# Kernel optimization log

Measured on AMD Instinct MI355X. Metric: run time of the kernel, lower is better.

Reference implementation:

```python
import jax, jax.numpy as jnp
import numpy as np

Q_MAX = 127.0  # 2**(8-1) - 1

def _quant_per_tensor_absmax(t):
    # scale = clamp(absmax, 1e-5) / 127 ; q = round(t / scale)
    scale = jnp.maximum(jnp.max(jnp.abs(t)), 1e-5) / Q_MAX
    q = jnp.round(t / scale)
    return q, scale

def setup_inputs() -> dict:
    key = jax.random.key(0)
    k1, k2, k3 = jax.random.split(key, 3)
    B, S, IN, OUT = 4, 2048, 4096, 4096
    x = jax.random.normal(k1, (B, S, IN), dtype=jnp.float32)
    weight = jax.random.normal(k2, (OUT, IN), dtype=jnp.float32)
    bias = jax.random.normal(k3, (1, OUT), dtype=jnp.float32)
    return {"x": x, "weight": weight, "bias": bias}

def reference(x, weight, bias):
    # per-tensor weight quantization (done at from_float time in the original)
    q_w, s_w = _quant_per_tensor_absmax(weight)   # q_w: [OUT, IN] integer-valued
    # per-tensor activation quantization (forward path)
    q_x, s_x = _quant_per_tensor_absmax(x)        # q_x: [B, S, IN] integer-valued
    # int8 GEMM (simulated in fp32: values are small integers) + fused dequant
    y = jnp.einsum('bsi,oi->bso', q_x, q_w)       # [B, S, OUT]
    y = y * (s_x * s_w) + bias                    # dequant scale + bias
    return y
```

## Files before the change

### kernel.cpp

```cpp
#include <hip/hip_runtime.h>
#include <hip/hip_bf16.h>
#include <stdint.h>

#define M_DIM 8192
#define N_DIM 4096
#define K_DIM 4096

typedef int i32x4 __attribute__((ext_vector_type(4)));

#define NB_X 2048
#define NB_W 1024
#define NB_TOT (NB_X + NB_W)

__global__ void w8a8_absmax_kernel(const float* __restrict__ x,
                                   const float* __restrict__ w,
                                   float* __restrict__ partials) {
    int b = blockIdx.x;
    const float4* p;
    int n8, bi, nb;
    if (b < NB_X) { p = (const float4*)x; n8 = (M_DIM * K_DIM) / 8; bi = b;        nb = NB_X; }
    else          { p = (const float4*)w; n8 = (N_DIM * K_DIM) / 8; bi = b - NB_X; nb = NB_W; }

    float m = 0.f;
    int stride = nb * 256;
    for (int i = bi * 256 + threadIdx.x; i < n8; i += stride) {
        float4 v0 = p[2 * i];
        float4 v1 = p[2 * i + 1];
        float m0 = fmaxf(fmaxf(fabsf(v0.x), fabsf(v0.y)), fmaxf(fabsf(v0.z), fabsf(v0.w)));
        float m1 = fmaxf(fmaxf(fabsf(v1.x), fabsf(v1.y)), fmaxf(fabsf(v1.z), fabsf(v1.w)));
        m = fmaxf(m, fmaxf(m0, m1));
    }
    #pragma unroll
    for (int o = 32; o > 0; o >>= 1)
        m = fmaxf(m, __shfl_xor(m, o, 64));

    __shared__ float red[4];
    if ((threadIdx.x & 63) == 0) red[threadIdx.x >> 6] = m;
    __syncthreads();
    if (threadIdx.x == 0)
        partials[b] = fmaxf(fmaxf(red[0], red[1]), fmaxf(red[2], red[3]));
}

__global__ void w8a8_finalize_kernel(const float* __restrict__ partials,
                                     float* __restrict__ finals) {
    int base = (blockIdx.x == 0) ? 0 : NB_X;
    int n    = (blockIdx.x == 0) ? NB_X : NB_W;
    float m = 0.f;
    for (int i = threadIdx.x; i < n; i += 256)
        m = fmaxf(m, partials[base + i]);
    #pragma unroll
    for (int o = 32; o > 0; o >>= 1)
        m = fmaxf(m, __shfl_xor(m, o, 64));
    __shared__ float red[4];
    if ((threadIdx.x & 63) == 0) red[threadIdx.x >> 6] = m;
    __syncthreads();
    if (threadIdx.x == 0) {
        m = fmaxf(fmaxf(red[0], red[1]), fmaxf(red[2], red[3]));
        finals[blockIdx.x] = fmaxf(m, 1e-5f) / 127.0f;
    }
}

__global__ void w8a8_quant_kernel(const float* __restrict__ x,
                                  const float* __restrict__ w,
                                  uint2* __restrict__ qx,
                                  uint2* __restrict__ qw,
                                  const float* __restrict__ finals) {
    int b = blockIdx.x;
    const float4* in4;
    uint2* outq;
    int n8, bi, nb;
    float scale;
    if (b < NB_X) { in4 = (const float4*)x; outq = qx; n8 = (M_DIM * K_DIM) / 8; bi = b;        nb = NB_X; scale = finals[0]; }
    else          { in4 = (const float4*)w; outq = qw; n8 = (N_DIM * K_DIM) / 8; bi = b - NB_X; nb = NB_W; scale = finals[1]; }

    int stride = nb * 256;
    for (int i = bi * 256 + threadIdx.x; i < n8; i += stride) {
        float4 v0 = in4[2 * i];
        float4 v1 = in4[2 * i + 1];
        int a0 = (int)rintf(v0.x / scale), a1 = (int)rintf(v0.y / scale);
        int a2 = (int)rintf(v0.z / scale), a3 = (int)rintf(v0.w / scale);
        int a4 = (int)rintf(v1.x / scale), a5 = (int)rintf(v1.y / scale);
        int a6 = (int)rintf(v1.z / scale), a7 = (int)rintf(v1.w / scale);
        uint2 o;
        o.x = (unsigned)(a0 & 0xff) | ((unsigned)(a1 & 0xff) << 8) |
              ((unsigned)(a2 & 0xff) << 16) | ((unsigned)(a3 & 0xff) << 24);
        o.y = (unsigned)(a4 & 0xff) | ((unsigned)(a5 & 0xff) << 8) |
              ((unsigned)(a6 & 0xff) << 16) | ((unsigned)(a7 & 0xff) << 24);
        outq[i] = o;
    }
}

#define BM 256
#define BN 256
#define BK 128
#define NT (K_DIM / BK)
#define NTN (N_DIM / BN)
#define LDS_BUF 65536

#define STAGE_A(BUF, MH, KT) do {                                              \
    _Pragma("unroll")                                                          \
    for (int r_ = 0; r_ < 2; ++r_)                                             \
        __builtin_amdgcn_global_load_lds(                                      \
            (const __attribute__((address_space(1))) void*)(a_base + (size_t)((KT) + goffA[MH][r_])), \
            (__attribute__((address_space(3))) void*)(lds + (BUF)*LDS_BUF + (MH)*16384 + ldst[r_]),   \
            16, 0, 0);                                                         \
} while (0)

#define STAGE_B(BUF, NH, KT) do {                                              \
    _Pragma("unroll")                                                          \
    for (int r_ = 0; r_ < 2; ++r_)                                             \
        __builtin_amdgcn_global_load_lds(                                      \
            (const __attribute__((address_space(1))) void*)(b_base + (size_t)((KT) + goffB[NH][r_])), \
            (__attribute__((address_space(3))) void*)(lds + (BUF)*LDS_BUF + 32768 + (NH)*16384 + ldst[r_]), \
            16, 0, 0);                                                         \
} while (0)

#define RA_A(BUF, MH, DST) do {                                                \
    _Pragma("unroll")                                                          \
    for (int m4_ = 0; m4_ < 4; ++m4_) {                                        \
        DST[m4_][0] = *(const i32x4*)(lds + (BUF)*LDS_BUF + (MH)*16384 + laneA + m4_*2048 + koff[0]); \
        DST[m4_][1] = *(const i32x4*)(lds + (BUF)*LDS_BUF + (MH)*16384 + laneA + m4_*2048 + koff[1]); \
    }                                                                          \
} while (0)

#define RA_B(BUF, NH, DST) do {                                                \
    _Pragma("unroll")                                                          \
    for (int n1_ = 0; n1_ < 2; ++n1_) {                                        \
        DST[n1_][0] = *(const i32x4*)(lds + (BUF)*LDS_BUF + 32768 + (NH)*16384 + laneB + n1_*2048 + koff[0]); \
        DST[n1_][1] = *(const i32x4*)(lds + (BUF)*LDS_BUF + 32768 + (NH)*16384 + laneB + n1_*2048 + koff[1]); \
    }                                                                          \
} while (0)

#define MMA4(MH, NH, AARR, BARR) do {                                          \
    __builtin_amdgcn_s_setprio(1);                                             \
    _Pragma("unroll")                                                          \
    for (int m4_ = 0; m4_ < 4; ++m4_) {                                        \
        _Pragma("unroll")                                                      \
        for (int n1_ = 0; n1_ < 2; ++n1_) {                                    \
            i32x4 c_ = acc[(MH)*4 + m4_][(NH)*2 + n1_];                        \
            c_ = __builtin_amdgcn_mfma_i32_16x16x64_i8(AARR[m4_][0], BARR[n1_][0], c_, 0, 0, 0); \
            c_ = __builtin_amdgcn_mfma_i32_16x16x64_i8(AARR[m4_][1], BARR[n1_][1], c_, 0, 0, 0); \
            acc[(MH)*4 + m4_][(NH)*2 + n1_] = c_;                              \
        }                                                                      \
    }                                                                          \
    __builtin_amdgcn_s_setprio(0);                                             \
} while (0)

#define BAR() __builtin_amdgcn_s_barrier()
#define SB0() __builtin_amdgcn_sched_barrier(0)
#define VMW(N) asm volatile("s_waitcnt vmcnt(" #N ")" ::: "memory")
#define LGKM(N) asm volatile("s_waitcnt lgkmcnt(" #N ")" ::: "memory")

#define TILE_BODY(BUF, OBUF, KT2, B0C, B0N) do {                               \
                                              \
    RA_B(BUF, 1, bB1);                                                         \
    SB0(); LGKM(4); SB0();                   \
    MMA4(0, 0, aA0, B0C);                                                      \
    BAR();                                                                     \
              \
    STAGE_A(BUF, 0, KT2); STAGE_B(BUF, 0, KT2);                                \
    RA_A(BUF, 1, aA1);                                                         \
    SB0(); LGKM(8); SB0();                             \
    MMA4(0, 1, aA0, bB1);                                                      \
    BAR();                                                                     \
     \
    STAGE_B(BUF, 1, KT2);                                                      \
    SB0(); LGKM(0); SB0();                                        \
    MMA4(1, 1, aA1, bB1);                                                      \
    SB0(); VMW(6);                       \
    BAR();                                \
     \
    RA_A(OBUF, 0, aA0); RA_B(OBUF, 0, B0N);                                    \
    STAGE_A(BUF, 1, KT2);                                                      \
    SB0();                                       \
    MMA4(1, 0, aA1, B0C);                                                      \
    BAR();                                                                     \
} while (0)

__global__ __launch_bounds__(512, 1) void w8a8_gemm_kernel(
    const signed char* __restrict__ qa,
    const signed char* __restrict__ qb,
    const float* __restrict__ bias,
    const float* __restrict__ finals,
    float* __restrict__ out)
{
    __shared__ __align__(16) char lds[2 * LDS_BUF];

    int t    = threadIdx.x;
    int lane = t & 63;
    int wid  = t >> 6;
    int wm   = wid >> 2;
    int wn   = wid & 3;
    int fr   = lane & 15;
    int fg   = lane >> 4;
    int frb2 = (fr >> 2) & 1;

    int bid = blockIdx.x;
    int cpx = gridDim.x >> 3;
    int swz = (bid & 7) * cpx + (bid >> 3);
    int tm = swz / NTN;
    int tn = swz % NTN;

    const signed char* a_base = qa + (size_t)tm * BM * K_DIM;
    const signed char* b_base = qb + (size_t)tn * BN * K_DIM;

    int goffA[2][2], goffB[2][2], ldst[2];
    #pragma unroll
    for (int r = 0; r < 2; ++r) {
        int unit = r * 512 + t;
        int sl   = unit >> 3;
        int c    = unit & 7;
        int cs   = c ^ (sl & 7);
        int rowA = (sl & 63) + ((sl >> 6) & 1) * 128;
        goffA[0][r] = rowA * K_DIM + cs * 16;
        goffA[1][r] = (rowA + 64) * K_DIM + cs * 16;
        int rowB = ((sl >> 5) & 3) * 64 + (sl & 31);
        goffB[0][r] = rowB * K_DIM + cs * 16;
        goffB[1][r] = (rowB + 32) * K_DIM + cs * 16;
        ldst[r] = r * 8192 + t * 16;
    }

    int laneA = (wm * 64 + fr) * 128 + (fg ^ (fr & 3)) * 16;
    int laneB = (wn * 32 + fr) * 128 + (fg ^ (fr & 3)) * 16;
    int koff[2];
    koff[0] = frb2 * 64;
    koff[1] = 64 - frb2 * 64;

    i32x4 acc[8][4] = {};
    i32x4 aA0[4][2], aA1[4][2], bB1[2][2], bB0a[2][2], bB0b[2][2];

    STAGE_A(0, 0, 0);  STAGE_A(0, 1, 0);  STAGE_B(0, 0, 0);  STAGE_B(0, 1, 0);
    STAGE_A(1, 0, BK); STAGE_A(1, 1, BK); STAGE_B(1, 0, BK); STAGE_B(1, 1, BK);
    VMW(8);
    BAR();
    RA_A(0, 0, aA0); RA_B(0, 0, bB0a);

    #pragma unroll 1
    for (int it = 0; it < NT / 2; ++it) {
        int kt2 = ((2 * it + 2) & (NT - 1)) * BK;
        int kt3 = ((2 * it + 3) & (NT - 1)) * BK;
        TILE_BODY(0, 1, kt2, bB0a, bB0b);
        TILE_BODY(1, 0, kt3, bB0b, bB0a);
    }
    asm volatile("s_waitcnt vmcnt(0) lgkmcnt(0)" ::: "memory");
    BAR();

    float sprod = finals[0] * finals[1];
    int orow0 = tm * BM + wm * 128 + fg * 4;
    int ocol0 = tn * BN + wn * 64 + fr;
    #pragma unroll
    for (int n = 0; n < 4; ++n) {
        int col = ocol0 + n * 16;
        float bv = bias[col];
        #pragma unroll
        for (int m = 0; m < 8; ++m) {
            int row = orow0 + m * 16;
            #pragma unroll
            for (int rr = 0; rr < 4; ++rr) {
                out[(size_t)(row + rr) * N_DIM + col] = (float)acc[m][n][rr] * sprod + bv;
            }
        }
    }
}

extern "C" void kernel_launch(void* const* d_in, const int* in_sizes, int n_in,
                              void* d_out, int out_size, void* d_ws, size_t ws_size,
                              hipStream_t stream) {
    const float* x    = (const float*)d_in[0];
    const float* wgt  = (const float*)d_in[1];
    const float* bias = (const float*)d_in[2];
    float* out = (float*)d_out;

    char* ws = (char*)d_ws;
    float* finals   = (float*)ws;
    float* partials = (float*)(ws + 256);
    signed char* qx = (signed char*)(ws + 16384);
    signed char* qw = qx + (size_t)M_DIM * K_DIM;

    w8a8_absmax_kernel<<<NB_TOT, 256, 0, stream>>>(x, wgt, partials);
    w8a8_finalize_kernel<<<2, 256, 0, stream>>>(partials, finals);
    w8a8_quant_kernel<<<NB_TOT, 256, 0, stream>>>(x, wgt, (uint2*)qx, (uint2*)qw, finals);
    w8a8_gemm_kernel<<<(M_DIM / BM) * (N_DIM / BN), 512, 0, stream>>>(qx, qw, bias, finals, out);
}
```

Measured before the change: 216.1 us.

## Use 4 waves with 128x128 warp tiles and simplified two-phase K pipeline

Reworks the int8 GEMM from 8 waves with 128x64 per-wave tiles to 4 waves each computing a 128x128 output tile. Each wave now holds an 8x8 accumulator grid, and each half-K step is a single 64-MFMA batch. The four-phase interleaved staging schedule is replaced by a simpler one: read half-K fragments, run the MMA, barrier, stage the next tile, barrier. The aim is more register-level reuse and fewer LDS reads per MFMA, at the cost of much higher register pressure and less overlap of loads with compute.

```diff
diff --git a/kernel.cpp b/kernel.cpp
--- a/kernel.cpp
+++ b/kernel.cpp
@@ -97,51 +97,35 @@
 #define NTN (N_DIM / BN)
 #define LDS_BUF 65536
 
-#define STAGE_A(BUF, MH, KT) do {                                              \
-    _Pragma("unroll")                                                          \
-    for (int r_ = 0; r_ < 2; ++r_)                                             \
+#define STAGE_T(BUF, KT) do {                                                  \
+    _Pragma("unroll")                                                          \
+    for (int r_ = 0; r_ < 8; ++r_) {                                           \
         __builtin_amdgcn_global_load_lds(                                      \
-            (const __attribute__((address_space(1))) void*)(a_base + (size_t)((KT) + goffA[MH][r_])), \
-            (__attribute__((address_space(3))) void*)(lds + (BUF)*LDS_BUF + (MH)*16384 + ldst[r_]),   \
-            16, 0, 0);                                                         \
-} while (0)
-
-#define STAGE_B(BUF, NH, KT) do {                                              \
-    _Pragma("unroll")                                                          \
-    for (int r_ = 0; r_ < 2; ++r_)                                             \
+            (const __attribute__((address_space(1))) void*)(a_base + (size_t)(KT) + sgOff + (size_t)r_ * 131072), \
+            (__attribute__((address_space(3))) void*)(lds + (BUF)*LDS_BUF + stLds + r_*4096), 16, 0, 0); \
         __builtin_amdgcn_global_load_lds(                                      \
-            (const __attribute__((address_space(1))) void*)(b_base + (size_t)((KT) + goffB[NH][r_])), \
-            (__attribute__((address_space(3))) void*)(lds + (BUF)*LDS_BUF + 32768 + (NH)*16384 + ldst[r_]), \
-            16, 0, 0);                                                         \
-} while (0)
-
-#define RA_A(BUF, MH, DST) do {                                                \
-    _Pragma("unroll")                                                          \
-    for (int m4_ = 0; m4_ < 4; ++m4_) {                                        \
-        DST[m4_][0] = *(const i32x4*)(lds + (BUF)*LDS_BUF + (MH)*16384 + laneA + m4_*2048 + koff[0]); \
-        DST[m4_][1] = *(const i32x4*)(lds + (BUF)*LDS_BUF + (MH)*16384 + laneA + m4_*2048 + koff[1]); \
+            (const __attribute__((address_space(1))) void*)(b_base + (size_t)(KT) + sgOff + (size_t)r_ * 131072), \
+            (__attribute__((address_space(3))) void*)(lds + (BUF)*LDS_BUF + 32768 + stLds + r_*4096), 16, 0, 0); \
     }                                                                          \
 } while (0)
 
-#define RA_B(BUF, NH, DST) do {                                                \
-    _Pragma("unroll")                                                          \
-    for (int n1_ = 0; n1_ < 2; ++n1_) {                                        \
-        DST[n1_][0] = *(const i32x4*)(lds + (BUF)*LDS_BUF + 32768 + (NH)*16384 + laneB + n1_*2048 + koff[0]); \
-        DST[n1_][1] = *(const i32x4*)(lds + (BUF)*LDS_BUF + 32768 + (NH)*16384 + laneB + n1_*2048 + koff[1]); \
-    }                                                                          \
-} while (0)
-
-#define MMA4(MH, NH, AARR, BARR) do {                                          \
+#define RD_K(BUF, H, AS, BS) do {                                              \
+    _Pragma("unroll")                                                          \
+    for (int m_ = 0; m_ < 8; ++m_)                                             \
+        AS[m_] = *(const i32x4*)(lds + (BUF)*LDS_BUF + rdA + m_*2048 + koff[H]); \
+    _Pragma("unroll")                                                          \
+    for (int n_ = 0; n_ < 8; ++n_)                                             \
+        BS[n_] = *(const i32x4*)(lds + (BUF)*LDS_BUF + 32768 + rdB + n_*2048 + koff[H]); \
+} while (0)
+
+#define MMA64(AS, BS) do {                                                     \
     __builtin_amdgcn_s_setprio(1);                                             \
     _Pragma("unroll")                                                          \
-    for (int m4_ = 0; m4_ < 4; ++m4_) {                                        \
+    for (int m_ = 0; m_ < 8; ++m_) {                                           \
         _Pragma("unroll")                                                      \
-        for (int n1_ = 0; n1_ < 2; ++n1_) {                                    \
-            i32x4 c_ = acc[(MH)*4 + m4_][(NH)*2 + n1_];                        \
-            c_ = __builtin_amdgcn_mfma_i32_16x16x64_i8(AARR[m4_][0], BARR[n1_][0], c_, 0, 0, 0); \
-            c_ = __builtin_amdgcn_mfma_i32_16x16x64_i8(AARR[m4_][1], BARR[n1_][1], c_, 0, 0, 0); \
-            acc[(MH)*4 + m4_][(NH)*2 + n1_] = c_;                              \
-        }                                                                      \
+        for (int n_ = 0; n_ < 8; ++n_)                                         \
+            acc[m_][n_] = __builtin_amdgcn_mfma_i32_16x16x64_i8(               \
+                AS[m_], BS[n_], acc[m_][n_], 0, 0, 0);                         \
     }                                                                          \
     __builtin_amdgcn_s_setprio(0);                                             \
 } while (0)
@@ -151,33 +135,23 @@
 #define VMW(N) asm volatile("s_waitcnt vmcnt(" #N ")" ::: "memory")
 #define LGKM(N) asm volatile("s_waitcnt lgkmcnt(" #N ")" ::: "memory")
 
-#define TILE_BODY(BUF, OBUF, KT2, B0C, B0N) do {                               \
-                                              \
-    RA_B(BUF, 1, bB1);                                                         \
-    SB0(); LGKM(4); SB0();                   \
-    MMA4(0, 0, aA0, B0C);                                                      \
-    BAR();                                                                     \
-              \
-    STAGE_A(BUF, 0, KT2); STAGE_B(BUF, 0, KT2);                                \
-    RA_A(BUF, 1, aA1);                                                         \
-    SB0(); LGKM(8); SB0();                             \
-    MMA4(0, 1, aA0, bB1);                                                      \
-    BAR();                                                                     \
+#define TILE_BODY(X, Y, KT2) do {                                              \
      \
-    STAGE_B(BUF, 1, KT2);                                                      \
-    SB0(); LGKM(0); SB0();                                        \
-    MMA4(1, 1, aA1, bB1);                                                      \
-    SB0(); VMW(6);                       \
-    BAR();                                \
+    RD_K(X, 1, aS1, bS1);                                                      \
+    SB0(); LGKM(15); SB0();                                                    \
+    MMA64(aS0, bS0);                                                           \
      \
-    RA_A(OBUF, 0, aA0); RA_B(OBUF, 0, B0N);                                    \
-    STAGE_A(BUF, 1, KT2);                                                      \
-    SB0();                                       \
-    MMA4(1, 0, aA1, B0C);                                                      \
-    BAR();                                                                     \
-} while (0)
-
-__global__ __launch_bounds__(512, 1) void w8a8_gemm_kernel(
+    SB0(); LGKM(0); SB0();                                                     \
+    BAR();                                       \
+    STAGE_T(X, KT2);                                                           \
+    VMW(16); SB0();                  \
+    BAR();                                             \
+    RD_K(Y, 0, aS0, bS0);                                                      \
+    SB0();                                                                     \
+    MMA64(aS1, bS1);                                                           \
+} while (0)
+
+__global__ __launch_bounds__(256, 1) void w8a8_gemm_kernel(
     const signed char* __restrict__ qa,
     const signed char* __restrict__ qb,
     const float* __restrict__ bias,
@@ -189,11 +163,10 @@
     int t    = threadIdx.x;
     int lane = t & 63;
     int wid  = t >> 6;
-    int wm   = wid >> 2;
-    int wn   = wid & 3;
+    int wm   = wid >> 1;
+    int wn   = wid & 1;
     int fr   = lane & 15;
     int fg   = lane >> 4;
-    int frb2 = (fr >> 2) & 1;
 
     int bid = blockIdx.x;
     int cpx = gridDim.x >> 3;
@@ -204,52 +177,39 @@
     const signed char* a_base = qa + (size_t)tm * BM * K_DIM;
     const signed char* b_base = qb + (size_t)tn * BN * K_DIM;
 
-    int goffA[2][2], goffB[2][2], ldst[2];
-    #pragma unroll
-    for (int r = 0; r < 2; ++r) {
-        int unit = r * 512 + t;
-        int sl   = unit >> 3;
-        int c    = unit & 7;
-        int cs   = c ^ (sl & 7);
-        int rowA = (sl & 63) + ((sl >> 6) & 1) * 128;
-        goffA[0][r] = rowA * K_DIM + cs * 16;
-        goffA[1][r] = (rowA + 64) * K_DIM + cs * 16;
-        int rowB = ((sl >> 5) & 3) * 64 + (sl & 31);
-        goffB[0][r] = rowB * K_DIM + cs * 16;
-        goffB[1][r] = (rowB + 32) * K_DIM + cs * 16;
-        ldst[r] = r * 8192 + t * 16;
-    }
-
-    int laneA = (wm * 64 + fr) * 128 + (fg ^ (fr & 3)) * 16;
-    int laneB = (wn * 32 + fr) * 128 + (fg ^ (fr & 3)) * 16;
+    int sgOff = ((t >> 3) * K_DIM) + (((t & 7) ^ ((t >> 3) & 7)) << 4);
+    int stLds = t << 4;
+
+    int rdA = (wm * 128 + fr) * 128;
+    int rdB = (wn * 128 + fr) * 128;
     int koff[2];
-    koff[0] = frb2 * 64;
-    koff[1] = 64 - frb2 * 64;
-
-    i32x4 acc[8][4] = {};
-    i32x4 aA0[4][2], aA1[4][2], bB1[2][2], bB0a[2][2], bB0b[2][2];
-
-    STAGE_A(0, 0, 0);  STAGE_A(0, 1, 0);  STAGE_B(0, 0, 0);  STAGE_B(0, 1, 0);
-    STAGE_A(1, 0, BK); STAGE_A(1, 1, BK); STAGE_B(1, 0, BK); STAGE_B(1, 1, BK);
-    VMW(8);
+    koff[0] = ((fg ^ (fr & 7)) << 4);
+    koff[1] = (((4 | fg) ^ (fr & 7)) << 4);
+
+    i32x4 acc[8][8] = {};
+    i32x4 aS0[8], bS0[8], aS1[8], bS1[8];
+
+    STAGE_T(0, 0);
+    STAGE_T(1, BK);
+    VMW(16);
     BAR();
-    RA_A(0, 0, aA0); RA_B(0, 0, bB0a);
+    RD_K(0, 0, aS0, bS0);
 
     #pragma unroll 1
     for (int it = 0; it < NT / 2; ++it) {
         int kt2 = ((2 * it + 2) & (NT - 1)) * BK;
         int kt3 = ((2 * it + 3) & (NT - 1)) * BK;
-        TILE_BODY(0, 1, kt2, bB0a, bB0b);
-        TILE_BODY(1, 0, kt3, bB0b, bB0a);
+        TILE_BODY(0, 1, kt2);
+        TILE_BODY(1, 0, kt3);
     }
     asm volatile("s_waitcnt vmcnt(0) lgkmcnt(0)" ::: "memory");
     BAR();
 
     float sprod = finals[0] * finals[1];
     int orow0 = tm * BM + wm * 128 + fg * 4;
-    int ocol0 = tn * BN + wn * 64 + fr;
+    int ocol0 = tn * BN + wn * 128 + fr;
     #pragma unroll
-    for (int n = 0; n < 4; ++n) {
+    for (int n = 0; n < 8; ++n) {
         int col = ocol0 + n * 16;
         float bv = bias[col];
         #pragma unroll
@@ -280,5 +240,5 @@
     w8a8_absmax_kernel<<<NB_TOT, 256, 0, stream>>>(x, wgt, partials);
     w8a8_finalize_kernel<<<2, 256, 0, stream>>>(partials, finals);
     w8a8_quant_kernel<<<NB_TOT, 256, 0, stream>>>(x, wgt, (uint2*)qx, (uint2*)qw, finals);
-    w8a8_gemm_kernel<<<(M_DIM / BM) * (N_DIM / BN), 512, 0, stream>>>(qx, qw, bias, finals, out);
-}
+    w8a8_gemm_kernel<<<(M_DIM / BM) * (N_DIM / BN), 256, 0, stream>>>(qx, qw, bias, finals, out);
+}
```

Result: slower. 662.3 us (+206.5%).
